# Kernel optimization log

Measured on AMD Instinct MI355X. Metric: run time of the kernel, lower is better.

## Reference

```python
import jax, jax.numpy as jnp
import numpy as np

N_NODES = 100000
N_EDGES = 200000
Z_DIM = 64
ATTR_DIM = 768
HID = 128
N_CLASSES = 5


def setup_inputs() -> dict:
    key = jax.random.key(0)
    ks = jax.random.split(key, 6)
    z = jax.random.normal(ks[0], (N_NODES, Z_DIM), dtype=jnp.float32)
    edge_index = jax.random.randint(ks[1], (2, N_EDGES), 0, N_NODES, dtype=jnp.int64)
    edge_attr = jax.random.normal(ks[2], (N_EDGES, ATTR_DIM), dtype=jnp.float32)
    W1 = jax.random.normal(ks[3], (ATTR_DIM + Z_DIM, HID), dtype=jnp.float32) * 0.02
    b1 = jnp.zeros((HID,), dtype=jnp.float32)
    W2 = jax.random.normal(ks[4], (HID, N_CLASSES), dtype=jnp.float32) * 0.02
    b2 = jnp.zeros((N_CLASSES,), dtype=jnp.float32)
    return {"z": z, "edge_index": edge_index, "edge_attr": edge_attr,
            "W1": W1, "b1": b1, "W2": W2, "b2": b2}


def reference(z, edge_index, edge_attr, W1, b1, W2, b2):
    # decode(): gather endpoint embeddings, elementwise product  [E, 64]
    node_rep = z[edge_index[0]] * z[edge_index[1]]
    # concat with edge attributes -> [E, 64 + 768] (torch cat order: node_rep first)
    joint = jnp.concatenate([node_rep, edge_attr], axis=-1)
    # 2-layer MLP + softmax
    h = jax.nn.relu(joint @ W1 + b1)
    logits = h @ W2 + b2
    return jax.nn.softmax(logits, axis=-1)
```

## Files before the change

kernel.cpp:

```cpp
#include <hip/hip_runtime.h>
#include <hip/hip_bf16.h>

#define E_TOT 200000
#define NZ 64
#define ATTR_D 768
#define KD 832
#define HID_D 128
#define NCLS 5
#define NAT 24

typedef __attribute__((ext_vector_type(8))) short short8;
typedef __attribute__((ext_vector_type(4))) float f32x4;

typedef __attribute__((address_space(3))) unsigned       lds_u32_t;
typedef const __attribute__((address_space(1))) unsigned glob_u32_t;

__device__ __forceinline__ unsigned pk2(float a, float b) {
    __hip_bfloat162 h = __float22bfloat162_rn(make_float2(a, b));
    return *reinterpret_cast<unsigned*>(&h);
}

__device__ __forceinline__ short8 pack8(const float4 x0, const float4 x1) {
    union { unsigned u[4]; short8 s; } r;
    r.u[0] = pk2(x0.x, x0.y);
    r.u[1] = pk2(x0.z, x0.w);
    r.u[2] = pk2(x1.x, x1.y);
    r.u[3] = pk2(x1.z, x1.w);
    return r.s;
}

__global__ void prep_w1f(const float* __restrict__ W1, __hip_bfloat16* __restrict__ w1f) {
    int idx = blockIdx.x * 256 + threadIdx.x;
    if (idx >= 26 * 8 * 64 * 8) return;
    int j    = idx & 7;
    int lane = (idx >> 3) & 63;
    int f    = (idx >> 9) & 7;
    int kt   = idx >> 12;
    int n = f * 16 + (lane & 15);
    int k = kt * 32 + (lane >> 4) * 8 + j;
    w1f[idx] = __float2bfloat16(W1[(size_t)k * HID_D + n]);
}

__global__ __launch_bounds__(256, 2) void gcn_main(
    const float* __restrict__ z, const int* __restrict__ ei,
    const float* __restrict__ attr, const __hip_bfloat16* __restrict__ w1f,
    const float* __restrict__ b1, const float* __restrict__ W2,
    const float* __restrict__ b2, float* __restrict__ out) {

    __shared__ float As[2][128 * 32];

    const int t    = threadIdx.x;
    const int wv   = t >> 6;
    const int lane = t & 63;
    const int g    = lane >> 4;
    const int c0   = lane & 15;
    const int e0   = blockIdx.x * 128;

    const float* sbase[4];
#pragma unroll
    for (int i = 0; i < 4; ++i) {
        int L   = wv * 1024 + i * 4096 + lane * 16;
        int row = L >> 7;
        int p   = (L >> 4) & 7;
        int c   = p ^ (row & 7);
        int er  = e0 + row; if (er >= E_TOT) er = E_TOT - 1;
        sbase[i] = attr + (size_t)er * ATTR_D + c * 4;
    }

    auto STAGE = [&](int buf, int at) {
#pragma unroll
        for (int i = 0; i < 4; ++i) {
            __builtin_amdgcn_global_load_lds(
                (glob_u32_t*)(sbase[i] + at * 32),
                (lds_u32_t*)&As[buf][wv * 256 + i * 1024],
                16, 0, 0);
        }
    };

    const __hip_bfloat16* wf = w1f + (size_t)lane * 8;
    auto LOADB = [&](int kt, short8(&b)[8]) {
#pragma unroll
        for (int f = 0; f < 8; ++f)
            b[f] = *reinterpret_cast<const short8*>(wf + (size_t)(kt * 8 + f) * 512);
    };

    const float* zsp[2];
    const float* zdp[2];
#pragma unroll
    for (int m = 0; m < 2; ++m) {
        int e = e0 + wv * 32 + m * 16 + c0; if (e >= E_TOT) e = E_TOT - 1;
        int si = ei[e];
        int di = ei[E_TOT + e];
        zsp[m] = z + (size_t)si * NZ + g * 8;
        zdp[m] = z + (size_t)di * NZ + g * 8;
    }

    f32x4 acc[2][8];
#pragma unroll
    for (int m = 0; m < 2; ++m)
#pragma unroll
        for (int f = 0; f < 8; ++f) acc[m][f] = (f32x4){0.f, 0.f, 0.f, 0.f};

    STAGE(0, 0);

    {
        short8 bz0[8], bz1[8];
        LOADB(0, bz0);
        LOADB(1, bz1);
#pragma unroll
        for (int kt = 0; kt < 2; ++kt) {
            short8 a[2];
#pragma unroll
            for (int m = 0; m < 2; ++m) {
                const float4* ps = reinterpret_cast<const float4*>(zsp[m] + kt * 32);
                const float4* pd = reinterpret_cast<const float4*>(zdp[m] + kt * 32);
                float4 s0 = ps[0], s1 = ps[1];
                float4 d0 = pd[0], d1 = pd[1];
                float4 x0 = make_float4(s0.x * d0.x, s0.y * d0.y, s0.z * d0.z, s0.w * d0.w);
                float4 x1 = make_float4(s1.x * d1.x, s1.y * d1.y, s1.z * d1.z, s1.w * d1.w);
                a[m] = pack8(x0, x1);
            }
#pragma unroll
            for (int f = 0; f < 8; ++f) {
                short8 bb = kt ? bz1[f] : bz0[f];
                acc[0][f] = __builtin_amdgcn_mfma_f32_16x16x32_bf16(a[0], bb, acc[0][f], 0, 0, 0);
                acc[1][f] = __builtin_amdgcn_mfma_f32_16x16x32_bf16(a[1], bb, acc[1][f], 0, 0, 0);
            }
        }
    }

    short8 bC[8], bN[8];
    LOADB(2, bC);
    __syncthreads();

    for (int at = 0; at < NAT; ++at) {
        const int cur = at & 1;
        if (at + 1 < NAT) STAGE(cur ^ 1, at + 1);
        const int ktn = (at + 3 <= 25) ? at + 3 : 25;
        LOADB(ktn, bN);

        short8 a[2];
#pragma unroll
        for (int m = 0; m < 2; ++m) {
            int r    = wv * 32 + m * 16 + c0;
            int base = r * 32;
            int p0   = ((g * 2)     ^ (r & 7)) * 4;
            int p1   = ((g * 2 + 1) ^ (r & 7)) * 4;
            float4 x0 = *reinterpret_cast<const float4*>(&As[cur][base + p0]);
            float4 x1 = *reinterpret_cast<const float4*>(&As[cur][base + p1]);
            a[m] = pack8(x0, x1);
        }
#pragma unroll
        for (int f = 0; f < 8; ++f) {
            acc[0][f] = __builtin_amdgcn_mfma_f32_16x16x32_bf16(a[0], bC[f], acc[0][f], 0, 0, 0);
            acc[1][f] = __builtin_amdgcn_mfma_f32_16x16x32_bf16(a[1], bC[f], acc[1][f], 0, 0, 0);
        }
        __syncthreads();
#pragma unroll
        for (int f = 0; f < 8; ++f) bC[f] = bN[f];
    }

    float b1v[8], w2v[8][NCLS];
#pragma unroll
    for (int f = 0; f < 8; ++f) {
        int col = f * 16 + c0;
        b1v[f] = b1[col];
#pragma unroll
        for (int cc = 0; cc < NCLS; ++cc) w2v[f][cc] = W2[col * NCLS + cc];
    }
    float b2v[NCLS];
#pragma unroll
    for (int cc = 0; cc < NCLS; ++cc) b2v[cc] = b2[cc];

#pragma unroll
    for (int m = 0; m < 2; ++m) {
#pragma unroll
        for (int i = 0; i < 4; ++i) {
            float lg[NCLS] = {0.f, 0.f, 0.f, 0.f, 0.f};
#pragma unroll
            for (int f = 0; f < 8; ++f) {
                float h = acc[m][f][i] + b1v[f];
                h = fmaxf(h, 0.f);
#pragma unroll
                for (int cc = 0; cc < NCLS; ++cc) lg[cc] = fmaf(h, w2v[f][cc], lg[cc]);
            }
#pragma unroll
            for (int mask = 1; mask < 16; mask <<= 1) {
#pragma unroll
                for (int cc = 0; cc < NCLS; ++cc) lg[cc] += __shfl_xor(lg[cc], mask);
            }
#pragma unroll
            for (int cc = 0; cc < NCLS; ++cc) lg[cc] += b2v[cc];

            float mx = fmaxf(fmaxf(fmaxf(lg[0], lg[1]), fmaxf(lg[2], lg[3])), lg[4]);
            float q[NCLS];
            float s = 0.f;
#pragma unroll
            for (int cc = 0; cc < NCLS; ++cc) { q[cc] = __expf(lg[cc] - mx); s += q[cc]; }
            float inv = 1.0f / s;
            float num = (c0 == 0) ? q[0] : (c0 == 1) ? q[1] : (c0 == 2) ? q[2]
                      : (c0 == 3) ? q[3] : q[4];
            int rowl = wv * 32 + m * 16 + g * 4 + i;
            int eo = e0 + rowl;
            if (eo < E_TOT && c0 < NCLS) out[(size_t)eo * NCLS + c0] = num * inv;
        }
    }
}

extern "C" void kernel_launch(void* const* d_in, const int* in_sizes, int n_in,
                              void* d_out, int out_size, void* d_ws, size_t ws_size,
                              hipStream_t stream) {
    const float* z    = (const float*)d_in[0];
    const int*   ei   = (const int*)d_in[1];
    const float* attr = (const float*)d_in[2];
    const float* W1   = (const float*)d_in[3];
    const float* b1   = (const float*)d_in[4];
    const float* W2   = (const float*)d_in[5];
    const float* b2   = (const float*)d_in[6];
    float* out = (float*)d_out;
    __hip_bfloat16* w1f = (__hip_bfloat16*)d_ws;

    prep_w1f<<<(26 * 8 * 64 * 8 + 255) / 256, 256, 0, stream>>>(W1, w1f);
    const int nblk = (E_TOT + 127) / 128;
    gcn_main<<<nblk, 256, 0, stream>>>(z, ei, attr, w1f, b1, W2, b2, out);
}
```

Measured before the change: 174.5 us.

## Triple-buffer wave-private attribute tiles and replace block barriers with vmcnt waits

The LDS attribute staging is remapped so each wave loads exactly the 32 rows it later consumes. That makes the tiles wave-private, so the per-iteration __syncthreads is removed and an explicit s_waitcnt vmcnt(12) is used instead. The buffer count grows from two to three with a prefetch distance of two, and the main loop is unrolled by six with ping-pong B-fragment registers. The goal is to keep more global loads in flight and stop waves from stalling on each other. The cost is 50% more LDS per block and correctness that depends on hand-counted vmcnt values and on the compiler's instruction ordering.

```diff
diff --git a/kernel.cpp b/kernel.cpp
--- a/kernel.cpp
+++ b/kernel.cpp
@@ -47,7 +47,7 @@
     const float* __restrict__ b1, const float* __restrict__ W2,
     const float* __restrict__ b2, float* __restrict__ out) {
 
-    __shared__ float As[2][128 * 32];
+    __shared__ float As[3][128 * 32];
 
     const int t    = threadIdx.x;
     const int wv   = t >> 6;
@@ -59,7 +59,7 @@
     const float* sbase[4];
 #pragma unroll
     for (int i = 0; i < 4; ++i) {
-        int L   = wv * 1024 + i * 4096 + lane * 16;
+        int L   = wv * 4096 + i * 1024 + lane * 16;
         int row = L >> 7;
         int p   = (L >> 4) & 7;
         int c   = p ^ (row & 7);
@@ -67,12 +67,12 @@
         sbase[i] = attr + (size_t)er * ATTR_D + c * 4;
     }
 
-    auto STAGE = [&](int buf, int at) {
+    auto STAGE = [&](int buf, int s) {
 #pragma unroll
         for (int i = 0; i < 4; ++i) {
             __builtin_amdgcn_global_load_lds(
-                (glob_u32_t*)(sbase[i] + at * 32),
-                (lds_u32_t*)&As[buf][wv * 256 + i * 1024],
+                (glob_u32_t*)(sbase[i] + s * 32),
+                (lds_u32_t*)&As[buf][wv * 1024 + i * 256],
                 16, 0, 0);
         }
     };
@@ -101,7 +101,10 @@
 #pragma unroll
         for (int f = 0; f < 8; ++f) acc[m][f] = (f32x4){0.f, 0.f, 0.f, 0.f};
 
+    short8 bX[8], bY[8];
     STAGE(0, 0);
+    LOADB(2, bX);
+    STAGE(1, 1);
 
     {
         short8 bz0[8], bz1[8];
@@ -129,36 +132,41 @@
         }
     }
 
-    short8 bC[8], bN[8];
-    LOADB(2, bC);
-    __syncthreads();
-
-    for (int at = 0; at < NAT; ++at) {
-        const int cur = at & 1;
-        if (at + 1 < NAT) STAGE(cur ^ 1, at + 1);
-        const int ktn = (at + 3 <= 25) ? at + 3 : 25;
-        LOADB(ktn, bN);
-
-        short8 a[2];
-#pragma unroll
-        for (int m = 0; m < 2; ++m) {
-            int r    = wv * 32 + m * 16 + c0;
-            int base = r * 32;
-            int p0   = ((g * 2)     ^ (r & 7)) * 4;
-            int p1   = ((g * 2 + 1) ^ (r & 7)) * 4;
-            float4 x0 = *reinterpret_cast<const float4*>(&As[cur][base + p0]);
-            float4 x1 = *reinterpret_cast<const float4*>(&As[cur][base + p1]);
-            a[m] = pack8(x0, x1);
-        }
-#pragma unroll
-        for (int f = 0; f < 8; ++f) {
-            acc[0][f] = __builtin_amdgcn_mfma_f32_16x16x32_bf16(a[0], bC[f], acc[0][f], 0, 0, 0);
-            acc[1][f] = __builtin_amdgcn_mfma_f32_16x16x32_bf16(a[1], bC[f], acc[1][f], 0, 0, 0);
-        }
-        __syncthreads();
-#pragma unroll
-        for (int f = 0; f < 8; ++f) bC[f] = bN[f];
-    }
+#define STEP(AT, BUF, BCUR, BNXT)                                              \
+    {                                                                          \
+        asm volatile("s_waitcnt vmcnt(12)" ::: "memory");                      \
+        __builtin_amdgcn_sched_barrier(0);                                     \
+        const float* Ab = &As[BUF][0];                                         \
+        int r0  = wv * 32 + c0;                                                \
+        int r1  = r0 + 16;                                                     \
+        int p00 = ((g * 2)     ^ (r0 & 7)) * 4;                                \
+        int p01 = ((g * 2 + 1) ^ (r0 & 7)) * 4;                                \
+        int p10 = ((g * 2)     ^ (r1 & 7)) * 4;                                \
+        int p11 = ((g * 2 + 1) ^ (r1 & 7)) * 4;                                \
+        float4 x00 = *reinterpret_cast<const float4*>(Ab + r0 * 32 + p00);     \
+        float4 x01 = *reinterpret_cast<const float4*>(Ab + r0 * 32 + p01);     \
+        float4 x10 = *reinterpret_cast<const float4*>(Ab + r1 * 32 + p10);     \
+        float4 x11 = *reinterpret_cast<const float4*>(Ab + r1 * 32 + p11);     \
+        LOADB(((AT) + 3 > 25 ? 25 : (AT) + 3), BNXT);                          \
+        STAGE(((AT) + 2) % 3, ((AT) + 2 > 23 ? 23 : (AT) + 2));                \
+        short8 a0 = pack8(x00, x01);                                           \
+        short8 a1 = pack8(x10, x11);                                           \
+        _Pragma("unroll")                                                      \
+        for (int f = 0; f < 8; ++f) {                                          \
+            acc[0][f] = __builtin_amdgcn_mfma_f32_16x16x32_bf16(a0, BCUR[f], acc[0][f], 0, 0, 0); \
+            acc[1][f] = __builtin_amdgcn_mfma_f32_16x16x32_bf16(a1, BCUR[f], acc[1][f], 0, 0, 0); \
+        }                                                                      \
+    }
+
+    for (int at = 0; at < NAT; at += 6) {
+        STEP(at + 0, 0, bX, bY)
+        STEP(at + 1, 1, bY, bX)
+        STEP(at + 2, 2, bX, bY)
+        STEP(at + 3, 0, bY, bX)
+        STEP(at + 4, 1, bX, bY)
+        STEP(at + 5, 2, bY, bX)
+    }
+#undef STEP
 
     float b1v[8], w2v[8][NCLS];
 #pragma unroll
```

Result: slower. 187.2 us (+7.3%).

## Shrink edge tile to 64 rows and stage 128-wide K chunks with explicit waitcnt

Applied to the files above, without the earlier changes.

Each block now handles 64 edges instead of 128 (one 16-row MFMA tile per wave), and the attribute K loop stages 128 columns per step over 6 stages instead of 32 columns over 24. Each stage loads four K-subtiles of W1 fragments and overlaps the next global-to-LDS copy, using sched_barriers and a manual vmcnt wait in place of per-step __syncthreads. The goal is fewer barriers, more bytes in flight, and more blocks for occupancy. The cost is half the reuse of each W1 fragment, more B registers (4x8 short8), and dropped bounds clamps that rely on E being divisible by 64.

```diff
diff --git a/kernel.cpp b/kernel.cpp
--- a/kernel.cpp
+++ b/kernel.cpp
@@ -4,10 +4,11 @@
 #define E_TOT 200000
 #define NZ 64
 #define ATTR_D 768
-#define KD 832
 #define HID_D 128
 #define NCLS 5
-#define NAT 24
+#define M_BLK 64
+#define BKF 128
+#define NST 6
 
 typedef __attribute__((ext_vector_type(8))) short short8;
 typedef __attribute__((ext_vector_type(4))) float f32x4;
@@ -47,32 +48,30 @@
     const float* __restrict__ b1, const float* __restrict__ W2,
     const float* __restrict__ b2, float* __restrict__ out) {
 
-    __shared__ float As[2][128 * 32];
+    __shared__ float As[2][M_BLK * BKF];
 
     const int t    = threadIdx.x;
     const int wv   = t >> 6;
     const int lane = t & 63;
     const int g    = lane >> 4;
     const int c0   = lane & 15;
-    const int e0   = blockIdx.x * 128;
-
-    const float* sbase[4];
-#pragma unroll
-    for (int i = 0; i < 4; ++i) {
-        int L   = wv * 1024 + i * 4096 + lane * 16;
-        int row = L >> 7;
-        int p   = (L >> 4) & 7;
-        int c   = p ^ (row & 7);
-        int er  = e0 + row; if (er >= E_TOT) er = E_TOT - 1;
-        sbase[i] = attr + (size_t)er * ATTR_D + c * 4;
-    }
-
-    auto STAGE = [&](int buf, int at) {
-#pragma unroll
-        for (int i = 0; i < 4; ++i) {
+    const int e0   = blockIdx.x * M_BLK;
+
+    const float* sbase[8];
+#pragma unroll
+    for (int i = 0; i < 8; ++i) {
+        int R  = wv * 16 + i * 2 + (lane >> 5);
+        int c  = (lane & 31) ^ (R & 31);
+        int ec = e0 + R;
+        sbase[i] = attr + (size_t)ec * ATTR_D + c * 4;
+    }
+
+    auto STAGE = [&](int buf, int s) {
+#pragma unroll
+        for (int i = 0; i < 8; ++i) {
             __builtin_amdgcn_global_load_lds(
-                (glob_u32_t*)(sbase[i] + at * 32),
-                (lds_u32_t*)&As[buf][wv * 256 + i * 1024],
+                (glob_u32_t*)(sbase[i] + s * BKF),
+                (lds_u32_t*)&As[buf][wv * 2048 + i * 256],
                 16, 0, 0);
         }
     };
@@ -84,80 +83,67 @@
             b[f] = *reinterpret_cast<const short8*>(wf + (size_t)(kt * 8 + f) * 512);
     };
 
-    const float* zsp[2];
-    const float* zdp[2];
-#pragma unroll
-    for (int m = 0; m < 2; ++m) {
-        int e = e0 + wv * 32 + m * 16 + c0; if (e >= E_TOT) e = E_TOT - 1;
-        int si = ei[e];
-        int di = ei[E_TOT + e];
-        zsp[m] = z + (size_t)si * NZ + g * 8;
-        zdp[m] = z + (size_t)di * NZ + g * 8;
-    }
-
-    f32x4 acc[2][8];
-#pragma unroll
-    for (int m = 0; m < 2; ++m)
-#pragma unroll
-        for (int f = 0; f < 8; ++f) acc[m][f] = (f32x4){0.f, 0.f, 0.f, 0.f};
+    const int e = e0 + wv * 16 + c0;
+    const float* zsp = z + (size_t)ei[e] * NZ + g * 8;
+    const float* zdp = z + (size_t)ei[E_TOT + e] * NZ + g * 8;
+
+    f32x4 acc[8];
+#pragma unroll
+    for (int f = 0; f < 8; ++f) acc[f] = (f32x4){0.f, 0.f, 0.f, 0.f};
 
     STAGE(0, 0);
-
     {
         short8 bz0[8], bz1[8];
         LOADB(0, bz0);
         LOADB(1, bz1);
 #pragma unroll
         for (int kt = 0; kt < 2; ++kt) {
-            short8 a[2];
-#pragma unroll
-            for (int m = 0; m < 2; ++m) {
-                const float4* ps = reinterpret_cast<const float4*>(zsp[m] + kt * 32);
-                const float4* pd = reinterpret_cast<const float4*>(zdp[m] + kt * 32);
-                float4 s0 = ps[0], s1 = ps[1];
-                float4 d0 = pd[0], d1 = pd[1];
-                float4 x0 = make_float4(s0.x * d0.x, s0.y * d0.y, s0.z * d0.z, s0.w * d0.w);
-                float4 x1 = make_float4(s1.x * d1.x, s1.y * d1.y, s1.z * d1.z, s1.w * d1.w);
-                a[m] = pack8(x0, x1);
-            }
+            const float4* ps = reinterpret_cast<const float4*>(zsp + kt * 32);
+            const float4* pd = reinterpret_cast<const float4*>(zdp + kt * 32);
+            float4 s0 = ps[0], s1 = ps[1];
+            float4 d0 = pd[0], d1 = pd[1];
+            float4 x0 = make_float4(s0.x * d0.x, s0.y * d0.y, s0.z * d0.z, s0.w * d0.w);
+            float4 x1 = make_float4(s1.x * d1.x, s1.y * d1.y, s1.z * d1.z, s1.w * d1.w);
+            short8 a = pack8(x0, x1);
 #pragma unroll
             for (int f = 0; f < 8; ++f) {
                 short8 bb = kt ? bz1[f] : bz0[f];
-                acc[0][f] = __builtin_amdgcn_mfma_f32_16x16x32_bf16(a[0], bb, acc[0][f], 0, 0, 0);
-                acc[1][f] = __builtin_amdgcn_mfma_f32_16x16x32_bf16(a[1], bb, acc[1][f], 0, 0, 0);
+                acc[f] = __builtin_amdgcn_mfma_f32_16x16x32_bf16(a, bb, acc[f], 0, 0, 0);
             }
         }
     }
 
-    short8 bC[8], bN[8];
-    LOADB(2, bC);
-    __syncthreads();
-
-    for (int at = 0; at < NAT; ++at) {
-        const int cur = at & 1;
-        if (at + 1 < NAT) STAGE(cur ^ 1, at + 1);
-        const int ktn = (at + 3 <= 25) ? at + 3 : 25;
-        LOADB(ktn, bN);
-
-        short8 a[2];
-#pragma unroll
-        for (int m = 0; m < 2; ++m) {
-            int r    = wv * 32 + m * 16 + c0;
-            int base = r * 32;
-            int p0   = ((g * 2)     ^ (r & 7)) * 4;
-            int p1   = ((g * 2 + 1) ^ (r & 7)) * 4;
-            float4 x0 = *reinterpret_cast<const float4*>(&As[cur][base + p0]);
-            float4 x1 = *reinterpret_cast<const float4*>(&As[cur][base + p1]);
-            a[m] = pack8(x0, x1);
-        }
-#pragma unroll
-        for (int f = 0; f < 8; ++f) {
-            acc[0][f] = __builtin_amdgcn_mfma_f32_16x16x32_bf16(a[0], bC[f], acc[0][f], 0, 0, 0);
-            acc[1][f] = __builtin_amdgcn_mfma_f32_16x16x32_bf16(a[1], bC[f], acc[1][f], 0, 0, 0);
-        }
-        __syncthreads();
-#pragma unroll
-        for (int f = 0; f < 8; ++f) bC[f] = bN[f];
+    short8 bB[4][8];
+#pragma unroll
+    for (int s = 0; s < NST; ++s) {
+#pragma unroll
+        for (int sub = 0; sub < 4; ++sub)
+            LOADB(2 + s * 4 + sub, bB[sub]);
+        __builtin_amdgcn_sched_barrier(0);
+        if (s < NST - 1) {
+            STAGE((s + 1) & 1, s + 1);
+            __builtin_amdgcn_sched_barrier(0);
+            asm volatile("s_waitcnt vmcnt(8)" ::: "memory");
+        } else {
+            asm volatile("s_waitcnt vmcnt(0)" ::: "memory");
+        }
+        __builtin_amdgcn_sched_barrier(0);
+
+        const int buf = s & 1;
+        const int R31 = (wv * 16 + c0) & 31;
+        const int rbase = wv * 2048 + c0 * 128;
+#pragma unroll
+        for (int sub = 0; sub < 4; ++sub) {
+            int cc = sub * 8 + g * 2;
+            int p0 = cc ^ R31;
+            int p1 = (cc + 1) ^ R31;
+            float4 x0 = *reinterpret_cast<const float4*>(&As[buf][rbase + p0 * 4]);
+            float4 x1 = *reinterpret_cast<const float4*>(&As[buf][rbase + p1 * 4]);
+            short8 a = pack8(x0, x1);
+#pragma unroll
+            for (int f = 0; f < 8; ++f)
+                acc[f] = __builtin_amdgcn_mfma_f32_16x16x32_bf16(a, bB[sub][f], acc[f], 0, 0, 0);
+        }
     }
 
     float b1v[8], w2v[8][NCLS];
@@ -173,37 +159,33 @@
     for (int cc = 0; cc < NCLS; ++cc) b2v[cc] = b2[cc];
 
 #pragma unroll
-    for (int m = 0; m < 2; ++m) {
-#pragma unroll
-        for (int i = 0; i < 4; ++i) {
-            float lg[NCLS] = {0.f, 0.f, 0.f, 0.f, 0.f};
-#pragma unroll
-            for (int f = 0; f < 8; ++f) {
-                float h = acc[m][f][i] + b1v[f];
-                h = fmaxf(h, 0.f);
-#pragma unroll
-                for (int cc = 0; cc < NCLS; ++cc) lg[cc] = fmaf(h, w2v[f][cc], lg[cc]);
-            }
-#pragma unroll
-            for (int mask = 1; mask < 16; mask <<= 1) {
-#pragma unroll
-                for (int cc = 0; cc < NCLS; ++cc) lg[cc] += __shfl_xor(lg[cc], mask);
-            }
-#pragma unroll
-            for (int cc = 0; cc < NCLS; ++cc) lg[cc] += b2v[cc];
-
-            float mx = fmaxf(fmaxf(fmaxf(lg[0], lg[1]), fmaxf(lg[2], lg[3])), lg[4]);
-            float q[NCLS];
-            float s = 0.f;
-#pragma unroll
-            for (int cc = 0; cc < NCLS; ++cc) { q[cc] = __expf(lg[cc] - mx); s += q[cc]; }
-            float inv = 1.0f / s;
-            float num = (c0 == 0) ? q[0] : (c0 == 1) ? q[1] : (c0 == 2) ? q[2]
-                      : (c0 == 3) ? q[3] : q[4];
-            int rowl = wv * 32 + m * 16 + g * 4 + i;
-            int eo = e0 + rowl;
-            if (eo < E_TOT && c0 < NCLS) out[(size_t)eo * NCLS + c0] = num * inv;
-        }
+    for (int i = 0; i < 4; ++i) {
+        float lg[NCLS] = {0.f, 0.f, 0.f, 0.f, 0.f};
+#pragma unroll
+        for (int f = 0; f < 8; ++f) {
+            float h = acc[f][i] + b1v[f];
+            h = fmaxf(h, 0.f);
+#pragma unroll
+            for (int cc = 0; cc < NCLS; ++cc) lg[cc] = fmaf(h, w2v[f][cc], lg[cc]);
+        }
+#pragma unroll
+        for (int mask = 1; mask < 16; mask <<= 1) {
+#pragma unroll
+            for (int cc = 0; cc < NCLS; ++cc) lg[cc] += __shfl_xor(lg[cc], mask);
+        }
+#pragma unroll
+        for (int cc = 0; cc < NCLS; ++cc) lg[cc] += b2v[cc];
+
+        float mx = fmaxf(fmaxf(fmaxf(lg[0], lg[1]), fmaxf(lg[2], lg[3])), lg[4]);
+        float q[NCLS];
+        float ssum = 0.f;
+#pragma unroll
+        for (int cc = 0; cc < NCLS; ++cc) { q[cc] = __expf(lg[cc] - mx); ssum += q[cc]; }
+        float inv = 1.0f / ssum;
+        float num = (c0 == 0) ? q[0] : (c0 == 1) ? q[1] : (c0 == 2) ? q[2]
+                  : (c0 == 3) ? q[3] : q[4];
+        int eo = e0 + wv * 16 + g * 4 + i;
+        if (c0 < NCLS) out[(size_t)eo * NCLS + c0] = num * inv;
     }
 }
 
@@ -221,6 +203,6 @@
     __hip_bfloat16* w1f = (__hip_bfloat16*)d_ws;
 
     prep_w1f<<<(26 * 8 * 64 * 8 + 255) / 256, 256, 0, stream>>>(W1, w1f);
-    const int nblk = (E_TOT + 127) / 128;
+    const int nblk = E_TOT / M_BLK;
     gcn_main<<<nblk, 256, 0, stream>>>(z, ei, attr, w1f, b1, W2, b2, out);
 }
```

After: 206.9 us. +18.6%, slower.

## Deepen attr staging to 64-wide K tiles with explicit waitcnt pipeline

Applied to the files above, without the earlier changes.

Each stage now stages 64 attribute columns per row (12 stages instead of 24), with 8 async global-to-LDS loads per thread. The loop is fully unrolled with manual vmcnt/lgkmcnt waits and barriers, and it double-buffers B fragments across two register sets. The z gathers are hoisted ahead of staging. The goal is to halve barrier count and keep more HBM traffic in flight on this bandwidth-bound stream. In exchange it doubles LDS to 64KB per block, which may limit occupancy, and drops the XOR swizzle, which can cause bank conflicts.

```diff
diff --git a/kernel.cpp b/kernel.cpp
--- a/kernel.cpp
+++ b/kernel.cpp
@@ -4,10 +4,9 @@
 #define E_TOT 200000
 #define NZ 64
 #define ATTR_D 768
-#define KD 832
 #define HID_D 128
 #define NCLS 5
-#define NAT 24
+#define NSTG 12
 
 typedef __attribute__((ext_vector_type(8))) short short8;
 typedef __attribute__((ext_vector_type(4))) float f32x4;
@@ -47,7 +46,7 @@
     const float* __restrict__ b1, const float* __restrict__ W2,
     const float* __restrict__ b2, float* __restrict__ out) {
 
-    __shared__ float As[2][128 * 32];
+    __shared__ float As[2][128 * 64];
 
     const int t    = threadIdx.x;
     const int wv   = t >> 6;
@@ -56,25 +55,22 @@
     const int c0   = lane & 15;
     const int e0   = blockIdx.x * 128;
 
-    const float* sbase[4];
-#pragma unroll
-    for (int i = 0; i < 4; ++i) {
-        int L   = wv * 1024 + i * 4096 + lane * 16;
-        int row = L >> 7;
-        int p   = (L >> 4) & 7;
-        int c   = p ^ (row & 7);
+    const float* sbase[8];
+#pragma unroll
+    for (int i = 0; i < 8; ++i) {
+        int O   = wv * 1024 + i * 4096 + lane * 16;
+        int row = O >> 8;
+        int c   = (O >> 4) & 15;
         int er  = e0 + row; if (er >= E_TOT) er = E_TOT - 1;
         sbase[i] = attr + (size_t)er * ATTR_D + c * 4;
     }
-
-    auto STAGE = [&](int buf, int at) {
-#pragma unroll
-        for (int i = 0; i < 4; ++i) {
+    auto STAGE = [&](int buf, int s) {
+#pragma unroll
+        for (int i = 0; i < 8; ++i)
             __builtin_amdgcn_global_load_lds(
-                (glob_u32_t*)(sbase[i] + at * 32),
+                (glob_u32_t*)(sbase[i] + s * 64),
                 (lds_u32_t*)&As[buf][wv * 256 + i * 1024],
                 16, 0, 0);
-        }
     };
 
     const __hip_bfloat16* wf = w1f + (size_t)lane * 8;
@@ -84,81 +80,110 @@
             b[f] = *reinterpret_cast<const short8*>(wf + (size_t)(kt * 8 + f) * 512);
     };
 
+    f32x4 acc[2][8];
+#pragma unroll
+    for (int m = 0; m < 2; ++m)
+#pragma unroll
+        for (int f = 0; f < 8; ++f) acc[m][f] = (f32x4){0.f, 0.f, 0.f, 0.f};
+
     const float* zsp[2];
     const float* zdp[2];
 #pragma unroll
     for (int m = 0; m < 2; ++m) {
         int e = e0 + wv * 32 + m * 16 + c0; if (e >= E_TOT) e = E_TOT - 1;
-        int si = ei[e];
-        int di = ei[E_TOT + e];
-        zsp[m] = z + (size_t)si * NZ + g * 8;
-        zdp[m] = z + (size_t)di * NZ + g * 8;
-    }
-
-    f32x4 acc[2][8];
+        zsp[m] = z + (size_t)ei[e] * NZ + g * 8;
+        zdp[m] = z + (size_t)ei[E_TOT + e] * NZ + g * 8;
+    }
+    float4 zsr[2][2][2], zdr[2][2][2];
 #pragma unroll
     for (int m = 0; m < 2; ++m)
 #pragma unroll
-        for (int f = 0; f < 8; ++f) acc[m][f] = (f32x4){0.f, 0.f, 0.f, 0.f};
-
+        for (int kt = 0; kt < 2; ++kt)
+#pragma unroll
+            for (int h = 0; h < 2; ++h) {
+                zsr[m][kt][h] = *reinterpret_cast<const float4*>(zsp[m] + kt * 32 + h * 4);
+                zdr[m][kt][h] = *reinterpret_cast<const float4*>(zdp[m] + kt * 32 + h * 4);
+            }
+    short8 bz0[8], bz1[8];
+    LOADB(0, bz0); LOADB(1, bz1);
     STAGE(0, 0);
 
-    {
-        short8 bz0[8], bz1[8];
-        LOADB(0, bz0);
-        LOADB(1, bz1);
-#pragma unroll
-        for (int kt = 0; kt < 2; ++kt) {
-            short8 a[2];
-#pragma unroll
-            for (int m = 0; m < 2; ++m) {
-                const float4* ps = reinterpret_cast<const float4*>(zsp[m] + kt * 32);
-                const float4* pd = reinterpret_cast<const float4*>(zdp[m] + kt * 32);
-                float4 s0 = ps[0], s1 = ps[1];
-                float4 d0 = pd[0], d1 = pd[1];
-                float4 x0 = make_float4(s0.x * d0.x, s0.y * d0.y, s0.z * d0.z, s0.w * d0.w);
-                float4 x1 = make_float4(s1.x * d1.x, s1.y * d1.y, s1.z * d1.z, s1.w * d1.w);
-                a[m] = pack8(x0, x1);
-            }
-#pragma unroll
-            for (int f = 0; f < 8; ++f) {
-                short8 bb = kt ? bz1[f] : bz0[f];
-                acc[0][f] = __builtin_amdgcn_mfma_f32_16x16x32_bf16(a[0], bb, acc[0][f], 0, 0, 0);
-                acc[1][f] = __builtin_amdgcn_mfma_f32_16x16x32_bf16(a[1], bb, acc[1][f], 0, 0, 0);
-            }
-        }
-    }
-
-    short8 bC[8], bN[8];
-    LOADB(2, bC);
-    __syncthreads();
-
-    for (int at = 0; at < NAT; ++at) {
-        const int cur = at & 1;
-        if (at + 1 < NAT) STAGE(cur ^ 1, at + 1);
-        const int ktn = (at + 3 <= 25) ? at + 3 : 25;
-        LOADB(ktn, bN);
-
+#pragma unroll
+    for (int kt = 0; kt < 2; ++kt) {
         short8 a[2];
 #pragma unroll
         for (int m = 0; m < 2; ++m) {
-            int r    = wv * 32 + m * 16 + c0;
-            int base = r * 32;
-            int p0   = ((g * 2)     ^ (r & 7)) * 4;
-            int p1   = ((g * 2 + 1) ^ (r & 7)) * 4;
-            float4 x0 = *reinterpret_cast<const float4*>(&As[cur][base + p0]);
-            float4 x1 = *reinterpret_cast<const float4*>(&As[cur][base + p1]);
+            float4 x0, x1;
+            x0.x = zsr[m][kt][0].x * zdr[m][kt][0].x;
+            x0.y = zsr[m][kt][0].y * zdr[m][kt][0].y;
+            x0.z = zsr[m][kt][0].z * zdr[m][kt][0].z;
+            x0.w = zsr[m][kt][0].w * zdr[m][kt][0].w;
+            x1.x = zsr[m][kt][1].x * zdr[m][kt][1].x;
+            x1.y = zsr[m][kt][1].y * zdr[m][kt][1].y;
+            x1.z = zsr[m][kt][1].z * zdr[m][kt][1].z;
+            x1.w = zsr[m][kt][1].w * zdr[m][kt][1].w;
             a[m] = pack8(x0, x1);
         }
 #pragma unroll
         for (int f = 0; f < 8; ++f) {
-            acc[0][f] = __builtin_amdgcn_mfma_f32_16x16x32_bf16(a[0], bC[f], acc[0][f], 0, 0, 0);
-            acc[1][f] = __builtin_amdgcn_mfma_f32_16x16x32_bf16(a[1], bC[f], acc[1][f], 0, 0, 0);
+            short8 bb = kt ? bz1[f] : bz0[f];
+            acc[0][f] = __builtin_amdgcn_mfma_f32_16x16x32_bf16(a[0], bb, acc[0][f], 0, 0, 0);
+            acc[1][f] = __builtin_amdgcn_mfma_f32_16x16x32_bf16(a[1], bb, acc[1][f], 0, 0, 0);
         }
-        __syncthreads();
-#pragma unroll
-        for (int f = 0; f < 8; ++f) bC[f] = bN[f];
-    }
+    }
+
+    short8 bx0[8], bx1[8], by0[8], by1[8];
+    LOADB(2, bx0); LOADB(3, bx1);
+    STAGE(1, 1);
+
+#define ITER(S, BC0, BC1, BN0, BN1)                                            \
+    {                                                                          \
+        asm volatile("s_waitcnt vmcnt(8)" ::: "memory");                       \
+        __builtin_amdgcn_sched_barrier(0);                                     \
+        __builtin_amdgcn_s_barrier();                                          \
+        float4 x[2][2][2];                                                     \
+        _Pragma("unroll")                                                      \
+        for (int m = 0; m < 2; ++m) {                                          \
+            int r = wv * 32 + m * 16 + c0;                                     \
+            _Pragma("unroll")                                                  \
+            for (int kk = 0; kk < 2; ++kk) {                                   \
+                const float* p = &As[(S) & 1][r * 64 + kk * 32 + g * 8];       \
+                x[m][kk][0] = *reinterpret_cast<const float4*>(p);             \
+                x[m][kk][1] = *reinterpret_cast<const float4*>(p + 4);         \
+            }                                                                  \
+        }                                                                      \
+        asm volatile("s_waitcnt lgkmcnt(0)" ::: "memory");                     \
+        __builtin_amdgcn_sched_barrier(0);                                     \
+        __builtin_amdgcn_s_barrier();                                          \
+        if ((S) + 1 < NSTG) { LOADB(2 * (S) + 4, BN0); LOADB(2 * (S) + 5, BN1); } \
+        if ((S) + 2 < NSTG) STAGE((S) & 1, (S) + 2);                           \
+        __builtin_amdgcn_sched_barrier(0);                                     \
+        _Pragma("unroll")                                                      \
+        for (int kk = 0; kk < 2; ++kk) {                                       \
+            short8 a0 = pack8(x[0][kk][0], x[0][kk][1]);                       \
+            short8 a1 = pack8(x[1][kk][0], x[1][kk][1]);                       \
+            _Pragma("unroll")                                                  \
+            for (int f = 0; f < 8; ++f) {                                      \
+                short8 bb = kk ? (BC1)[f] : (BC0)[f];                          \
+                acc[0][f] = __builtin_amdgcn_mfma_f32_16x16x32_bf16(a0, bb, acc[0][f], 0, 0, 0); \
+                acc[1][f] = __builtin_amdgcn_mfma_f32_16x16x32_bf16(a1, bb, acc[1][f], 0, 0, 0); \
+            }                                                                  \
+        }                                                                      \
+    }
+
+    ITER(0,  bx0, bx1, by0, by1)
+    ITER(1,  by0, by1, bx0, bx1)
+    ITER(2,  bx0, bx1, by0, by1)
+    ITER(3,  by0, by1, bx0, bx1)
+    ITER(4,  bx0, bx1, by0, by1)
+    ITER(5,  by0, by1, bx0, bx1)
+    ITER(6,  bx0, bx1, by0, by1)
+    ITER(7,  by0, by1, bx0, bx1)
+    ITER(8,  bx0, bx1, by0, by1)
+    ITER(9,  by0, by1, bx0, bx1)
+    ITER(10, bx0, bx1, by0, by1)
+    ITER(11, by0, by1, bx0, bx1)
+#undef ITER
 
     float b1v[8], w2v[8][NCLS];
 #pragma unroll
@@ -200,8 +225,7 @@
             float inv = 1.0f / s;
             float num = (c0 == 0) ? q[0] : (c0 == 1) ? q[1] : (c0 == 2) ? q[2]
                       : (c0 == 3) ? q[3] : q[4];
-            int rowl = wv * 32 + m * 16 + g * 4 + i;
-            int eo = e0 + rowl;
+            int eo = e0 + wv * 32 + m * 16 + g * 4 + i;
             if (eo < E_TOT && c0 < NCLS) out[(size_t)eo * NCLS + c0] = num * inv;
         }
     }
```

Measured after the change: 195.9 us. 1.12x slower.
